# Kernel tuning notes

Hardware: AMD Instinct MI355X
Metric: run time of the kernel (lower is better)

## Reference

```python
import jax, jax.numpy as jnp
import numpy as np

ETA = 0.15
LAM = 0.05
K = 6


def setup_inputs() -> dict:
    key = jax.random.key(0)
    ks = jax.random.split(key, 9)
    Bsz, L, d, hidden = 32, 8192, 64, 256
    scale = lambda fan_in: 1.0 / np.sqrt(fan_in)
    return {
        "A": jax.random.normal(ks[0], (Bsz, L, d), jnp.float32),
        "B": jax.random.normal(ks[1], (Bsz, L, d), jnp.float32),
        "q": jax.random.normal(ks[2], (Bsz, L, d), jnp.float32),
        "W1": jax.random.normal(ks[3], (2 * d, hidden), jnp.float32) * scale(2 * d),
        "b1": jax.random.normal(ks[4], (hidden,), jnp.float32) * 0.01,
        "W2": jax.random.normal(ks[5], (hidden, d), jnp.float32) * scale(hidden),
        "b2": jax.random.normal(ks[6], (d,), jnp.float32) * 0.01,
        "Wq": jax.random.normal(ks[7], (d, d), jnp.float32) * scale(d),
        "bq": jax.random.normal(ks[8], (d,), jnp.float32) * 0.01,
    }


def _smooth1d(x):
    return x - LAM * (2.0 * x - jnp.roll(x, 1, axis=1) - jnp.roll(x, -1, axis=1))


def reference(A, B, q, W1, b1, W2, b2, Wq, bq):
    # mu_net: Linear -> ReLU -> Linear -> Softplus on concat([A,B])
    h = jnp.concatenate([A, B], axis=-1)  # [B, L, 2d]
    mu = jax.nn.softplus(jax.nn.relu(h @ W1 + b1) @ W2 + b2)  # [B, L, d]
    gate = jnp.tanh(q @ Wq + bq)
    mu = mu * (1.0 + 0.5 * gate)

    hA, hB = A, B
    for _ in range(K):
        step = ETA * (mu * (hA - hB))
        hA = _smooth1d(hA - step)
        hB = _smooth1d(hB + step)

    energy = 0.5 * jnp.sum(mu * jnp.square(hA - hB), axis=(1, 2))  # [B]
    return hA, hB, energy
```

## Files before the change

kernel.cpp:

```cpp
#include <hip/hip_runtime.h>
#include <hip/hip_fp16.h>

#define ETA 0.15f
#define LAM 0.05f

typedef unsigned int uint32;
typedef __attribute__((ext_vector_type(8))) short short8;
typedef __attribute__((ext_vector_type(4))) float floatx4;
typedef __attribute__((ext_vector_type(2))) uint32 uint32x2;
typedef __attribute__((ext_vector_type(4))) _Float16 half4;

static const int BSZ = 32, LL = 8192, DD = 64;
static const int RTOT = BSZ * LL;

static const size_t W1T_OFF = 0;
static const size_t W2T_OFF = W1T_OFF + 256 * 128 * 2;
static const size_t WQT_OFF = W2T_OFF + 64 * 256 * 2;

__device__ __forceinline__ unsigned short f2bf(float f) {
    uint32 u = __builtin_bit_cast(uint32, f);
    uint32 r = (u + 0x7FFFu + ((u >> 16) & 1u)) >> 16;
    return (unsigned short)r;
}
__device__ __forceinline__ uint32 cvtpk(float lo, float hi) {
    uint32 r;
    asm("v_cvt_pk_bf16_f32 %0, %1, %2" : "=v"(r) : "v"(lo), "v"(hi));
    return r;
}
__device__ __forceinline__ float fast_softplus(float x) {
    return fmaxf(x, 0.f) + __logf(1.f + __expf(-fabsf(x)));
}
__device__ __forceinline__ float fast_tanh(float x) {
    float t = __expf(-2.f * fabsf(x));
    float r = (1.f - t) / (1.f + t);
    return copysignf(r, x);
}

__global__ void prep_kernel(const float* __restrict__ W1, const float* __restrict__ W2,
                            const float* __restrict__ Wq,
                            unsigned short* __restrict__ w1t, unsigned short* __restrict__ w2t,
                            unsigned short* __restrict__ wqt, float* __restrict__ energy) {
    int tid = blockIdx.x * blockDim.x + threadIdx.x;
    int nth = gridDim.x * blockDim.x;
    for (int i = tid; i < 256 * 128; i += nth) { int n = i >> 7, k = i & 127; w1t[i] = f2bf(W1[k * 256 + n]); }
    for (int i = tid; i < 64 * 256; i += nth) { int n = i >> 8, k = i & 255; w2t[i] = f2bf(W2[k * 64 + n]); }
    for (int i = tid; i < 64 * 64;  i += nth) { int n = i >> 6, k = i & 63;  wqt[i] = f2bf(Wq[k * 64 + n]); }
    if (tid < 32) energy[tid] = 0.f;
}

__global__ __launch_bounds__(256, 2) void fused_kernel(
    const float* __restrict__ A, const float* __restrict__ B, const float* __restrict__ Q,
    const float* __restrict__ b1, const float* __restrict__ b2, const float* __restrict__ bq,
    const unsigned short* __restrict__ w1t, const unsigned short* __restrict__ w2t,
    const unsigned short* __restrict__ wqt,
    float* __restrict__ outA, float* __restrict__ outB, float* __restrict__ energy) {
    __shared__ char lds[64048];
    unsigned short* Xs = (unsigned short*)(lds);
    unsigned short* Qs = (unsigned short*)(lds + 21760);
    unsigned short* Zs = (unsigned short*)(lds + 21760);
    _Float16* muS = (_Float16*)(lds);
    float* exb = (float*)(lds + 11264);
    float* esm = (float*)(lds + 44032);

    const int tid = threadIdx.x;
    const int lane = tid & 63;
    const int w = tid >> 6;
    const int q4 = lane >> 4;
    const int l16 = lane & 15;
    const int g = tid >> 4;
    const int c4 = tid & 15;
    const int bb = blockIdx.y;
    const int s0 = blockIdx.x * 64;
    const size_t bbase = (size_t)bb * LL;

    short8 wqf[2];
#pragma unroll
    for (int kt = 0; kt < 2; kt++)
        wqf[kt] = *(const short8*)&wqt[(w * 16 + l16) * 64 + kt * 32 + q4 * 8];
    floatx4 b1q[4];
#pragma unroll
    for (int ht = 0; ht < 4; ht++) b1q[ht] = *(const floatx4*)&b1[w * 64 + ht * 16 + q4 * 4];
    const floatx4 b2q = *(const floatx4*)&b2[w * 16 + q4 * 4];
    const floatx4 bqq = *(const floatx4*)&bq[w * 16 + q4 * 4];

    floatx4 av[5], bv[5];
    uint32* Xu = (uint32*)Xs;
    uint32* Qu = (uint32*)Qs;
#pragma unroll
    for (int i = 0; i < 5; i++) {
        int wr = g * 5 + i;
        int gl = (s0 + wr + LL - 8) & (LL - 1);
        size_t base = (bbase + gl) * 64 + c4 * 4;
        av[i] = *(const floatx4*)(A + base);
        bv[i] = *(const floatx4*)(B + base);
        floatx4 qv = *(const floatx4*)(Q + base);
        uint32x2 ua; ua.x = cvtpk(av[i].x, av[i].y); ua.y = cvtpk(av[i].z, av[i].w);
        uint32x2 ub; ub.x = cvtpk(bv[i].x, bv[i].y); ub.y = cvtpk(bv[i].z, bv[i].w);
        uint32x2 uq; uq.x = cvtpk(qv.x, qv.y);       uq.y = cvtpk(qv.z, qv.w);
        *(uint32x2*)&Xu[wr * 68 + c4 * 2] = ua;
        *(uint32x2*)&Xu[wr * 68 + 32 + c4 * 2] = ub;
        *(uint32x2*)&Qu[wr * 36 + c4 * 2] = uq;
    }
    __syncthreads();

    floatx4 acc3[5];
#pragma unroll
    for (int nt = 0; nt < 5; nt++) acc3[nt] = (floatx4){0.f, 0.f, 0.f, 0.f};
    __builtin_amdgcn_s_setprio(1);
#pragma unroll
    for (int nt = 0; nt < 5; nt++)
#pragma unroll
        for (int kt = 0; kt < 2; kt++) {
            short8 aq = *(const short8*)&Qs[(nt * 16 + l16) * 72 + kt * 32 + q4 * 8];
            acc3[nt] = __builtin_amdgcn_mfma_f32_16x16x32_bf16(wqf[kt], aq, acc3[nt], 0, 0, 0);
        }
    __builtin_amdgcn_s_setprio(0);
    short8 ax[5][4];
#pragma unroll
    for (int nt = 0; nt < 5; nt++)
#pragma unroll
        for (int kt = 0; kt < 4; kt++)
            ax[nt][kt] = *(const short8*)&Xs[(nt * 16 + l16) * 136 + kt * 32 + q4 * 8];
    __syncthreads();

#pragma unroll
    for (int ht = 0; ht < 4; ht++) {
        short8 wf[4];
#pragma unroll
        for (int kt = 0; kt < 4; kt++)
            wf[kt] = *(const short8*)&w1t[(w * 64 + ht * 16 + l16) * 128 + kt * 32 + q4 * 8];
        floatx4 acc[5];
#pragma unroll
        for (int nt = 0; nt < 5; nt++) acc[nt] = (floatx4){0.f, 0.f, 0.f, 0.f};
        __builtin_amdgcn_s_setprio(1);
#pragma unroll
        for (int kt = 0; kt < 4; kt++)
#pragma unroll
            for (int nt = 0; nt < 5; nt++)
                acc[nt] = __builtin_amdgcn_mfma_f32_16x16x32_bf16(wf[kt], ax[nt][kt], acc[nt], 0, 0, 0);
        __builtin_amdgcn_s_setprio(0);
#pragma unroll
        for (int nt = 0; nt < 5; nt++) {
            float z0 = fmaxf(acc[nt][0] + b1q[ht].x, 0.f);
            float z1 = fmaxf(acc[nt][1] + b1q[ht].y, 0.f);
            float z2 = fmaxf(acc[nt][2] + b1q[ht].z, 0.f);
            float z3 = fmaxf(acc[nt][3] + b1q[ht].w, 0.f);
            uint32x2 uz; uz.x = cvtpk(z0, z1); uz.y = cvtpk(z2, z3);
            *(uint32x2*)&Zs[(nt * 16 + l16) * 264 + w * 64 + ht * 16 + q4 * 4] = uz;
        }
    }
    short8 w2f[8];
#pragma unroll
    for (int kt = 0; kt < 8; kt++)
        w2f[kt] = *(const short8*)&w2t[(w * 16 + l16) * 256 + kt * 32 + q4 * 8];
    __syncthreads();

    floatx4 acc2[5];
#pragma unroll
    for (int nt = 0; nt < 5; nt++) acc2[nt] = (floatx4){0.f, 0.f, 0.f, 0.f};
    __builtin_amdgcn_s_setprio(1);
#pragma unroll
    for (int nt = 0; nt < 5; nt++)
#pragma unroll
        for (int kt = 0; kt < 8; kt++) {
            short8 az = *(const short8*)&Zs[(nt * 16 + l16) * 264 + kt * 32 + q4 * 8];
            acc2[nt] = __builtin_amdgcn_mfma_f32_16x16x32_bf16(w2f[kt], az, acc2[nt], 0, 0, 0);
        }
    __builtin_amdgcn_s_setprio(0);
#pragma unroll
    for (int nt = 0; nt < 5; nt++) {
        half4 h;
#pragma unroll
        for (int r = 0; r < 4; r++) {
            float sp = fast_softplus(acc2[nt][r] + ((const float*)&b2q)[r]);
            float gt = fast_tanh(acc3[nt][r] + ((const float*)&bqq)[r]);
            h[r] = (_Float16)(sp * (1.f + 0.5f * gt));
        }
        *(half4*)&muS[(nt * 16 + l16) * 68 + w * 16 + q4 * 4] = h;
    }
    __syncthreads();

    floatx4 sv[5], dv[5], fv[5];
#pragma unroll
    for (int i = 0; i < 5; i++) {
        sv[i] = av[i] + bv[i];
        dv[i] = av[i] - bv[i];
        half4 m4 = *(const half4*)&muS[(g * 5 + i) * 68 + c4 * 4];
        fv[i] = 1.f - (2.f * ETA) * __builtin_convertvector(m4, floatx4);
    }
#define EX(p, t, gg) (exb + (((p) * 4 + (t)) * 16 + (gg)) * 64 + c4 * 4)
    for (int it = 0; it < 6; it++) {
#pragma unroll
        for (int i = 0; i < 5; i++) dv[i] *= fv[i];
        const int p = it & 1;
        *(floatx4*)EX(p, 0, g) = sv[0];
        *(floatx4*)EX(p, 1, g) = sv[4];
        *(floatx4*)EX(p, 2, g) = dv[0];
        *(floatx4*)EX(p, 3, g) = dv[4];
        __syncthreads();
        floatx4 sUp = (g > 0)  ? *(const floatx4*)EX(p, 1, g - 1) : sv[0];
        floatx4 sDn = (g < 15) ? *(const floatx4*)EX(p, 0, g + 1) : sv[4];
        floatx4 dUp = (g > 0)  ? *(const floatx4*)EX(p, 3, g - 1) : dv[0];
        floatx4 dDn = (g < 15) ? *(const floatx4*)EX(p, 2, g + 1) : dv[4];
        floatx4 prev = sUp, cur = sv[0];
#pragma unroll
        for (int i = 0; i < 5; i++) {
            floatx4 nxt = (i < 4) ? sv[i + 1] : sDn;
            sv[i] = cur - LAM * (2.f * cur - prev - nxt);
            prev = cur; cur = nxt;
        }
        prev = dUp; cur = dv[0];
#pragma unroll
        for (int i = 0; i < 5; i++) {
            floatx4 nxt = (i < 4) ? dv[i + 1] : dDn;
            dv[i] = cur - LAM * (2.f * cur - prev - nxt);
            prev = cur; cur = nxt;
        }
    }
#undef EX
    float e = 0.f;
#pragma unroll
    for (int i = 0; i < 5; i++) {
        int wr = g * 5 + i;
        if (wr >= 8 && wr < 72) {
            floatx4 d = dv[i];
            floatx4 qv = (1.f - fv[i]) * d * d;
            e += qv.x + qv.y + qv.z + qv.w;
            size_t gidx = (bbase + s0 + (wr - 8)) * 64 + c4 * 4;
            *(floatx4*)(outA + gidx) = (sv[i] + d) * 0.5f;
            *(floatx4*)(outB + gidx) = (sv[i] - d) * 0.5f;
        }
    }
    e *= 0.25f / ETA;
#pragma unroll
    for (int off = 32; off > 0; off >>= 1) e += __shfl_down(e, off, 64);
    if ((tid & 63) == 0) esm[tid >> 6] = e;
    __syncthreads();
    if (tid == 0) atomicAdd(energy + bb, esm[0] + esm[1] + esm[2] + esm[3]);
}

extern "C" void kernel_launch(void* const* d_in, const int* in_sizes, int n_in,
                              void* d_out, int out_size, void* d_ws, size_t ws_size,
                              hipStream_t stream) {
    const float* A  = (const float*)d_in[0];
    const float* B  = (const float*)d_in[1];
    const float* Q  = (const float*)d_in[2];
    const float* W1 = (const float*)d_in[3];
    const float* b1 = (const float*)d_in[4];
    const float* W2 = (const float*)d_in[5];
    const float* b2 = (const float*)d_in[6];
    const float* Wq = (const float*)d_in[7];
    const float* bq = (const float*)d_in[8];

    float* outA = (float*)d_out;
    float* outB = outA + (size_t)RTOT * 64;
    float* energy = outB + (size_t)RTOT * 64;

    char* ws = (char*)d_ws;
    unsigned short* w1t = (unsigned short*)(ws + W1T_OFF);
    unsigned short* w2t = (unsigned short*)(ws + W2T_OFF);
    unsigned short* wqt = (unsigned short*)(ws + WQT_OFF);

    hipLaunchKernelGGL(prep_kernel, dim3(64), dim3(256), 0, stream,
                       W1, W2, Wq, w1t, w2t, wqt, energy);
    hipLaunchKernelGGL(fused_kernel, dim3(LL / 64, BSZ), dim3(256), 0, stream,
                       A, B, Q, b1, b2, bq, w1t, w2t, wqt, outA, outB, energy);
}
```

Measured before the change: 346.6 us.

## Split MLP hidden dim into halves, cut LDS/registers, closed-form sum smoothing

Result: faster. 333.3 us (-3.8%).

```diff
diff --git a/kernel.cpp b/kernel.cpp
--- a/kernel.cpp
+++ b/kernel.cpp
@@ -12,6 +12,14 @@
 
 static const int BSZ = 32, LL = 8192, DD = 64;
 static const int RTOT = BSZ * LL;
+
+#define SC0 0.5811044375f
+#define SC1 0.182631375f
+#define SC2 0.024907734375f
+#define SC3 0.0018309375f
+#define SC4 7.603125e-5f
+#define SC5 1.6875e-6f
+#define SC6 1.5625e-8f
 
 static const size_t W1T_OFF = 0;
 static const size_t W2T_OFF = W1T_OFF + 256 * 128 * 2;
@@ -48,19 +56,20 @@
     if (tid < 32) energy[tid] = 0.f;
 }
 
-__global__ __launch_bounds__(256, 2) void fused_kernel(
+__global__ __launch_bounds__(256, 3) void fused_kernel(
     const float* __restrict__ A, const float* __restrict__ B, const float* __restrict__ Q,
     const float* __restrict__ b1, const float* __restrict__ b2, const float* __restrict__ bq,
     const unsigned short* __restrict__ w1t, const unsigned short* __restrict__ w2t,
     const unsigned short* __restrict__ wqt,
     float* __restrict__ outA, float* __restrict__ outB, float* __restrict__ energy) {
-    __shared__ char lds[64048];
+    __shared__ char lds[43584];
     unsigned short* Xs = (unsigned short*)(lds);
     unsigned short* Qs = (unsigned short*)(lds + 21760);
     unsigned short* Zs = (unsigned short*)(lds + 21760);
     _Float16* muS = (_Float16*)(lds);
-    float* exb = (float*)(lds + 11264);
-    float* esm = (float*)(lds + 44032);
+    float* exb = (float*)(lds + 10880);
+    float* sS  = (float*)(lds);
+    float* esm = (float*)(lds + 43520);
 
     const int tid = threadIdx.x;
     const int lane = tid & 63;
@@ -77,13 +86,9 @@
 #pragma unroll
     for (int kt = 0; kt < 2; kt++)
         wqf[kt] = *(const short8*)&wqt[(w * 16 + l16) * 64 + kt * 32 + q4 * 8];
-    floatx4 b1q[4];
-#pragma unroll
-    for (int ht = 0; ht < 4; ht++) b1q[ht] = *(const floatx4*)&b1[w * 64 + ht * 16 + q4 * 4];
     const floatx4 b2q = *(const floatx4*)&b2[w * 16 + q4 * 4];
     const floatx4 bqq = *(const floatx4*)&bq[w * 16 + q4 * 4];
 
-    floatx4 av[5], bv[5];
     uint32* Xu = (uint32*)Xs;
     uint32* Qu = (uint32*)Qs;
 #pragma unroll
@@ -91,12 +96,12 @@
         int wr = g * 5 + i;
         int gl = (s0 + wr + LL - 8) & (LL - 1);
         size_t base = (bbase + gl) * 64 + c4 * 4;
-        av[i] = *(const floatx4*)(A + base);
-        bv[i] = *(const floatx4*)(B + base);
+        floatx4 av = *(const floatx4*)(A + base);
+        floatx4 bv = *(const floatx4*)(B + base);
         floatx4 qv = *(const floatx4*)(Q + base);
-        uint32x2 ua; ua.x = cvtpk(av[i].x, av[i].y); ua.y = cvtpk(av[i].z, av[i].w);
-        uint32x2 ub; ub.x = cvtpk(bv[i].x, bv[i].y); ub.y = cvtpk(bv[i].z, bv[i].w);
-        uint32x2 uq; uq.x = cvtpk(qv.x, qv.y);       uq.y = cvtpk(qv.z, qv.w);
+        uint32x2 ua; ua.x = cvtpk(av.x, av.y); ua.y = cvtpk(av.z, av.w);
+        uint32x2 ub; ub.x = cvtpk(bv.x, bv.y); ub.y = cvtpk(bv.z, bv.w);
+        uint32x2 uq; uq.x = cvtpk(qv.x, qv.y); uq.y = cvtpk(qv.z, qv.w);
         *(uint32x2*)&Xu[wr * 68 + c4 * 2] = ua;
         *(uint32x2*)&Xu[wr * 68 + 32 + c4 * 2] = ub;
         *(uint32x2*)&Qu[wr * 36 + c4 * 2] = uq;
@@ -115,101 +120,101 @@
             acc3[nt] = __builtin_amdgcn_mfma_f32_16x16x32_bf16(wqf[kt], aq, acc3[nt], 0, 0, 0);
         }
     __builtin_amdgcn_s_setprio(0);
-    short8 ax[5][4];
-#pragma unroll
-    for (int nt = 0; nt < 5; nt++)
+    __syncthreads();
+
+    floatx4 acc2[5];
+#pragma unroll
+    for (int nt = 0; nt < 5; nt++) acc2[nt] = (floatx4){0.f, 0.f, 0.f, 0.f};
+#pragma unroll
+    for (int h = 0; h < 2; h++) {
+        short8 wf0[4], wf1[4];
+#pragma unroll
+        for (int kt = 0; kt < 4; kt++) {
+            wf0[kt] = *(const short8*)&w1t[(h * 128 + w * 32 + l16) * 128 + kt * 32 + q4 * 8];
+            wf1[kt] = *(const short8*)&w1t[(h * 128 + w * 32 + 16 + l16) * 128 + kt * 32 + q4 * 8];
+        }
+        floatx4 acc0[5], acc1[5];
+#pragma unroll
+        for (int nt = 0; nt < 5; nt++) {
+            acc0[nt] = (floatx4){0.f, 0.f, 0.f, 0.f};
+            acc1[nt] = (floatx4){0.f, 0.f, 0.f, 0.f};
+        }
+        __builtin_amdgcn_s_setprio(1);
 #pragma unroll
         for (int kt = 0; kt < 4; kt++)
-            ax[nt][kt] = *(const short8*)&Xs[(nt * 16 + l16) * 136 + kt * 32 + q4 * 8];
-    __syncthreads();
-
-#pragma unroll
-    for (int ht = 0; ht < 4; ht++) {
-        short8 wf[4];
+#pragma unroll
+            for (int nt = 0; nt < 5; nt++) {
+                short8 xf = *(const short8*)&Xs[(nt * 16 + l16) * 136 + kt * 32 + q4 * 8];
+                acc0[nt] = __builtin_amdgcn_mfma_f32_16x16x32_bf16(wf0[kt], xf, acc0[nt], 0, 0, 0);
+                acc1[nt] = __builtin_amdgcn_mfma_f32_16x16x32_bf16(wf1[kt], xf, acc1[nt], 0, 0, 0);
+            }
+        __builtin_amdgcn_s_setprio(0);
+        const floatx4 b1q0 = *(const floatx4*)&b1[h * 128 + w * 32 + q4 * 4];
+        const floatx4 b1q1 = *(const floatx4*)&b1[h * 128 + w * 32 + 16 + q4 * 4];
+#pragma unroll
+        for (int nt = 0; nt < 5; nt++) {
+            uint32x2 uz;
+            uz.x = cvtpk(fmaxf(acc0[nt][0] + b1q0.x, 0.f), fmaxf(acc0[nt][1] + b1q0.y, 0.f));
+            uz.y = cvtpk(fmaxf(acc0[nt][2] + b1q0.z, 0.f), fmaxf(acc0[nt][3] + b1q0.w, 0.f));
+            *(uint32x2*)&Zs[(nt * 16 + l16) * 136 + w * 32 + q4 * 4] = uz;
+            uz.x = cvtpk(fmaxf(acc1[nt][0] + b1q1.x, 0.f), fmaxf(acc1[nt][1] + b1q1.y, 0.f));
+            uz.y = cvtpk(fmaxf(acc1[nt][2] + b1q1.z, 0.f), fmaxf(acc1[nt][3] + b1q1.w, 0.f));
+            *(uint32x2*)&Zs[(nt * 16 + l16) * 136 + w * 32 + 16 + q4 * 4] = uz;
+        }
+        short8 w2f[4];
 #pragma unroll
         for (int kt = 0; kt < 4; kt++)
-            wf[kt] = *(const short8*)&w1t[(w * 64 + ht * 16 + l16) * 128 + kt * 32 + q4 * 8];
-        floatx4 acc[5];
-#pragma unroll
-        for (int nt = 0; nt < 5; nt++) acc[nt] = (floatx4){0.f, 0.f, 0.f, 0.f};
+            w2f[kt] = *(const short8*)&w2t[(w * 16 + l16) * 256 + h * 128 + kt * 32 + q4 * 8];
+        __syncthreads();
         __builtin_amdgcn_s_setprio(1);
 #pragma unroll
-        for (int kt = 0; kt < 4; kt++)
-#pragma unroll
-            for (int nt = 0; nt < 5; nt++)
-                acc[nt] = __builtin_amdgcn_mfma_f32_16x16x32_bf16(wf[kt], ax[nt][kt], acc[nt], 0, 0, 0);
+        for (int nt = 0; nt < 5; nt++)
+#pragma unroll
+            for (int kt = 0; kt < 4; kt++) {
+                short8 az = *(const short8*)&Zs[(nt * 16 + l16) * 136 + kt * 32 + q4 * 8];
+                acc2[nt] = __builtin_amdgcn_mfma_f32_16x16x32_bf16(w2f[kt], az, acc2[nt], 0, 0, 0);
+            }
         __builtin_amdgcn_s_setprio(0);
-#pragma unroll
-        for (int nt = 0; nt < 5; nt++) {
-            float z0 = fmaxf(acc[nt][0] + b1q[ht].x, 0.f);
-            float z1 = fmaxf(acc[nt][1] + b1q[ht].y, 0.f);
-            float z2 = fmaxf(acc[nt][2] + b1q[ht].z, 0.f);
-            float z3 = fmaxf(acc[nt][3] + b1q[ht].w, 0.f);
-            uint32x2 uz; uz.x = cvtpk(z0, z1); uz.y = cvtpk(z2, z3);
-            *(uint32x2*)&Zs[(nt * 16 + l16) * 264 + w * 64 + ht * 16 + q4 * 4] = uz;
-        }
-    }
-    short8 w2f[8];
-#pragma unroll
-    for (int kt = 0; kt < 8; kt++)
-        w2f[kt] = *(const short8*)&w2t[(w * 16 + l16) * 256 + kt * 32 + q4 * 8];
-    __syncthreads();
-
-    floatx4 acc2[5];
-#pragma unroll
-    for (int nt = 0; nt < 5; nt++) acc2[nt] = (floatx4){0.f, 0.f, 0.f, 0.f};
-    __builtin_amdgcn_s_setprio(1);
-#pragma unroll
-    for (int nt = 0; nt < 5; nt++)
-#pragma unroll
-        for (int kt = 0; kt < 8; kt++) {
-            short8 az = *(const short8*)&Zs[(nt * 16 + l16) * 264 + kt * 32 + q4 * 8];
-            acc2[nt] = __builtin_amdgcn_mfma_f32_16x16x32_bf16(w2f[kt], az, acc2[nt], 0, 0, 0);
-        }
-    __builtin_amdgcn_s_setprio(0);
+        if (h == 0) __syncthreads();
+    }
+
 #pragma unroll
     for (int nt = 0; nt < 5; nt++) {
-        half4 h;
+        half4 hm;
 #pragma unroll
         for (int r = 0; r < 4; r++) {
             float sp = fast_softplus(acc2[nt][r] + ((const float*)&b2q)[r]);
             float gt = fast_tanh(acc3[nt][r] + ((const float*)&bqq)[r]);
-            h[r] = (_Float16)(sp * (1.f + 0.5f * gt));
-        }
-        *(half4*)&muS[(nt * 16 + l16) * 68 + w * 16 + q4 * 4] = h;
+            hm[r] = (_Float16)(sp * (1.f + 0.5f * gt));
+        }
+        *(half4*)&muS[(nt * 16 + l16) * 68 + w * 16 + q4 * 4] = hm;
     }
     __syncthreads();
 
     floatx4 sv[5], dv[5], fv[5];
 #pragma unroll
     for (int i = 0; i < 5; i++) {
-        sv[i] = av[i] + bv[i];
-        dv[i] = av[i] - bv[i];
-        half4 m4 = *(const half4*)&muS[(g * 5 + i) * 68 + c4 * 4];
+        int wr = g * 5 + i;
+        int gl = (s0 + wr + LL - 8) & (LL - 1);
+        size_t base = (bbase + gl) * 64 + c4 * 4;
+        floatx4 av = *(const floatx4*)(A + base);
+        floatx4 bv = *(const floatx4*)(B + base);
+        sv[i] = av + bv;
+        dv[i] = av - bv;
+        half4 m4 = *(const half4*)&muS[wr * 68 + c4 * 4];
         fv[i] = 1.f - (2.f * ETA) * __builtin_convertvector(m4, floatx4);
     }
-#define EX(p, t, gg) (exb + (((p) * 4 + (t)) * 16 + (gg)) * 64 + c4 * 4)
+#define EXD(p, t, gg) (exb + (((p) * 2 + (t)) * 16 + (gg)) * 68 + c4 * 4)
     for (int it = 0; it < 6; it++) {
 #pragma unroll
         for (int i = 0; i < 5; i++) dv[i] *= fv[i];
         const int p = it & 1;
-        *(floatx4*)EX(p, 0, g) = sv[0];
-        *(floatx4*)EX(p, 1, g) = sv[4];
-        *(floatx4*)EX(p, 2, g) = dv[0];
-        *(floatx4*)EX(p, 3, g) = dv[4];
+        *(floatx4*)EXD(p, 0, g) = dv[0];
+        *(floatx4*)EXD(p, 1, g) = dv[4];
         __syncthreads();
-        floatx4 sUp = (g > 0)  ? *(const floatx4*)EX(p, 1, g - 1) : sv[0];
-        floatx4 sDn = (g < 15) ? *(const floatx4*)EX(p, 0, g + 1) : sv[4];
-        floatx4 dUp = (g > 0)  ? *(const floatx4*)EX(p, 3, g - 1) : dv[0];
-        floatx4 dDn = (g < 15) ? *(const floatx4*)EX(p, 2, g + 1) : dv[4];
-        floatx4 prev = sUp, cur = sv[0];
-#pragma unroll
-        for (int i = 0; i < 5; i++) {
-            floatx4 nxt = (i < 4) ? sv[i + 1] : sDn;
-            sv[i] = cur - LAM * (2.f * cur - prev - nxt);
-            prev = cur; cur = nxt;
-        }
-        prev = dUp; cur = dv[0];
+        floatx4 dUp = (g > 0)  ? *(const floatx4*)EXD(p, 1, g - 1) : dv[0];
+        floatx4 dDn = (g < 15) ? *(const floatx4*)EXD(p, 0, g + 1) : dv[4];
+        floatx4 prev = dUp, cur = dv[0];
 #pragma unroll
         for (int i = 0; i < 5; i++) {
             floatx4 nxt = (i < 4) ? dv[i + 1] : dDn;
@@ -217,7 +222,7 @@
             prev = cur; cur = nxt;
         }
     }
-#undef EX
+#undef EXD
     float e = 0.f;
 #pragma unroll
     for (int i = 0; i < 5; i++) {
@@ -226,12 +231,43 @@
             floatx4 d = dv[i];
             floatx4 qv = (1.f - fv[i]) * d * d;
             e += qv.x + qv.y + qv.z + qv.w;
+        }
+    }
+    e *= 0.25f / ETA;
+
+    __syncthreads();
+#pragma unroll
+    for (int i = 0; i < 5; i++)
+        *(floatx4*)&sS[(g * 5 + i) * 68 + c4 * 4] = sv[i];
+    __syncthreads();
+    floatx4 srow[17];
+    const int sbase = g * 5 - 6;
+#pragma unroll
+    for (int j = 0; j < 17; j++) {
+        int rr = min(max(sbase + j, 0), 79);
+        srow[j] = *(const floatx4*)&sS[rr * 68 + c4 * 4];
+    }
+#pragma unroll
+    for (int i = 0; i < 5; i++) {
+        floatx4 sm = SC0 * srow[i + 6];
+        sm += SC1 * (srow[i + 5] + srow[i + 7]);
+        sm += SC2 * (srow[i + 4] + srow[i + 8]);
+        sm += SC3 * (srow[i + 3] + srow[i + 9]);
+        sm += SC4 * (srow[i + 2] + srow[i + 10]);
+        sm += SC5 * (srow[i + 1] + srow[i + 11]);
+        sm += SC6 * (srow[i + 0] + srow[i + 12]);
+        sv[i] = sm;
+    }
+
+#pragma unroll
+    for (int i = 0; i < 5; i++) {
+        int wr = g * 5 + i;
+        if (wr >= 8 && wr < 72) {
             size_t gidx = (bbase + s0 + (wr - 8)) * 64 + c4 * 4;
-            *(floatx4*)(outA + gidx) = (sv[i] + d) * 0.5f;
-            *(floatx4*)(outB + gidx) = (sv[i] - d) * 0.5f;
-        }
-    }
-    e *= 0.25f / ETA;
+            *(floatx4*)(outA + gidx) = (sv[i] + dv[i]) * 0.5f;
+            *(floatx4*)(outB + gidx) = (sv[i] - dv[i]) * 0.5f;
+        }
+    }
 #pragma unroll
     for (int off = 32; off > 0; off >>= 1) e += __shfl_down(e, off, 64);
     if ((tid & 63) == 0) esm[tid >> 6] = e;
```
